# Performance work log

Hardware: AMD Instinct MI355X
Metric: run time of the kernel (lower is better)

## Reference

```python
import jax, jax.numpy as jnp
import numpy as np

IN_F = 4096
OUT_F = 4096
RANK = 8
ALPHA = 8
SCALE = ALPHA / RANK


def setup_inputs() -> dict:
    key = jax.random.key(0)
    kx, kw, kb, ka = jax.random.split(key, 4)
    x = jax.random.normal(kx, (4, 4096, IN_F), dtype=jnp.float32)
    # base frozen linear params (torch Linear default init style, any values ok)
    W = jax.random.normal(kw, (OUT_F, IN_F), dtype=jnp.float32) * (1.0 / np.sqrt(IN_F))
    b = jax.random.normal(kb, (OUT_F,), dtype=jnp.float32) * 0.01
    # lora_A: kaiming_uniform_(a=sqrt(5)) -> U(-bound, bound), bound = sqrt(6/((1+5)*in_f)) = 1/sqrt(in_f)
    bound = 1.0 / np.sqrt(IN_F)
    lora_A = jax.random.uniform(ka, (RANK, IN_F), dtype=jnp.float32, minval=-bound, maxval=bound)
    # lora_B initialized to zeros per module; use small random values so the LoRA path is exercised
    lora_B = jax.random.normal(jax.random.fold_in(key, 7), (OUT_F, RANK), dtype=jnp.float32) * 0.02
    return {"x": x, "W": W, "b": b, "lora_A": lora_A, "lora_B": lora_B}


def reference(x, W, b, lora_A, lora_B):
    # base: x @ W.T + b  [B,S,out_f]
    base = jnp.einsum("bsi,oi->bso", x, W) + b
    # low-rank path: (x @ A.T) @ B.T * scale
    xa = jnp.einsum("bsi,ri->bsr", x, lora_A)  # [B,S,r]
    lora = jnp.einsum("bsr,or->bso", xa, lora_B)
    return base + lora * SCALE
```

## Files before the change

kernel.cpp:

```cpp
#include <hip/hip_runtime.h>
#include <cstdint>

#define K_IN   4096
#define N_OUT  4096
#define M_ROWS 16384
#define RANK   8
#define LSCALE 1.0f
#define NT     64
#define ROWB   8192
#define AHALF  1048576

typedef __attribute__((ext_vector_type(8))) short  short8;
typedef __attribute__((ext_vector_type(4))) float  floatx4;

__device__ __forceinline__ unsigned short f2bf(float f) {
  uint32_t u = __float_as_uint(f);
  u += 0x7FFFu + ((u >> 16) & 1u);
  return (unsigned short)(u >> 16);
}

__global__ __launch_bounds__(256) void fold_w_kernel(
    const float* __restrict__ W, const float* __restrict__ lA,
    const float* __restrict__ lB, unsigned short* __restrict__ Weff) {
  int idx = blockIdx.x * 256 + threadIdx.x;
  int o = idx >> 10;
  int k = (idx & 1023) << 2;
  float4 w = *reinterpret_cast<const float4*>(W + (size_t)o * K_IN + k);
#pragma unroll
  for (int r = 0; r < RANK; ++r) {
    float s = LSCALE * lB[o * RANK + r];
    float4 a = *reinterpret_cast<const float4*>(lA + r * K_IN + k);
    w.x += s * a.x; w.y += s * a.y; w.z += s * a.z; w.w += s * a.w;
  }
  ushort4 p;
  p.x = f2bf(w.x); p.y = f2bf(w.y); p.z = f2bf(w.z); p.w = f2bf(w.w);
  *reinterpret_cast<ushort4*>(Weff + (size_t)o * K_IN + k) = p;
}

__global__ __launch_bounds__(256) void cvt_x_kernel(
    const float* __restrict__ x, unsigned short* __restrict__ xb) {
  size_t i = ((size_t)blockIdx.x * 256 + threadIdx.x) * 8;
  float4 a = *reinterpret_cast<const float4*>(x + i);
  float4 c = *reinterpret_cast<const float4*>(x + i + 4);
  uint4 v;
  v.x = (uint32_t)f2bf(a.x) | ((uint32_t)f2bf(a.y) << 16);
  v.y = (uint32_t)f2bf(a.z) | ((uint32_t)f2bf(a.w) << 16);
  v.z = (uint32_t)f2bf(c.x) | ((uint32_t)f2bf(c.y) << 16);
  v.w = (uint32_t)f2bf(c.z) | ((uint32_t)f2bf(c.w) << 16);
  *reinterpret_cast<uint4*>(xb + i) = v;
}

__device__ __forceinline__ void gload_lds16(const void* g, void* l) {
  __builtin_amdgcn_global_load_lds(
      (const __attribute__((address_space(1))) void*)g,
      (__attribute__((address_space(3))) void*)l, 16, 0, 0);
}

#define BAR() do { asm volatile("" ::: "memory");                         \
    __builtin_amdgcn_s_barrier();                                         \
    asm volatile("" ::: "memory"); } while (0)

#define DSR(DST, ADDR, IMM)                                               \
  asm volatile("ds_read_b128 %0, %1 offset:%2"                            \
               : "=v"(DST) : "v"(ADDR), "i"(IMM))
#define LGKM(N) do {                                                      \
    asm volatile("s_waitcnt lgkmcnt(" #N ")" ::: "memory");               \
    __builtin_amdgcn_sched_barrier(0); } while (0)
#define VMW(N) do {                                                       \
    asm volatile("s_waitcnt vmcnt(" #N ")" ::: "memory");                 \
    __builtin_amdgcn_sched_barrier(0); } while (0)

__global__ __launch_bounds__(512, 2) void gemm256_kernel(
    const unsigned short* __restrict__ Xb, const unsigned short* __restrict__ Wb,
    const float* __restrict__ bias, float* __restrict__ out) {
  __shared__ alignas(16) char lds[2 * 65536];

  const int tid  = threadIdx.x;
  const int wave = tid >> 6, lane = tid & 63;
  const int wr = wave >> 2, wc = wave & 3;
  const int l15 = lane & 15, sq = lane >> 4;

  int bx  = blockIdx.x;
  int sbx = (bx & 7) * 128 + (bx >> 3);
  const int mt = sbx >> 4;
  const int nt = sbx & 15;

  const int rstg = tid >> 3;
  const int cbst = (((tid & 7) ^ ((tid >> 3) & 7)) << 4);
  const char* aBase = (const char*)Xb + (size_t)(mt * 256 + rstg) * ROWB + cbst;
  const char* bBase = (const char*)Wb + (size_t)(nt * 256 + rstg) * ROWB + cbst;

#define STAGE_TH(TH, HH) do {                                             \
    const char* src_ = ((HH) < 2 ? aBase + (size_t)(HH) * AHALF           \
                                 : bBase + (size_t)((HH) - 2) * AHALF)    \
                       + (TH) * 128;                                      \
    char* dst_ = lds + ((TH) & 1) * 65536 + (HH) * 16384 + tid * 16;      \
    gload_lds16(src_, dst_);                                              \
    gload_lds16(src_ + (size_t)64 * ROWB, dst_ + 8192);                   \
  } while (0)

  const unsigned ldsb = (unsigned)(unsigned long long)
      (__attribute__((address_space(3))) char*)lds;
  const unsigned X = (unsigned)((l15 & 7) << 4);
  const unsigned aRow = ldsb + wr * 16384 + l15 * 128;
  const unsigned bRow = ldsb + (2 + (wc >> 1)) * 16384 + (wc & 1) * 8192
                        + l15 * 128;
  unsigned aCur0 = aRow + ((0u  + sq * 16) ^ X);
  unsigned aCur1 = aRow + ((64u + sq * 16) ^ X);
  unsigned bCur0 = bRow + ((0u  + sq * 16) ^ X);
  unsigned bCur1 = bRow + ((64u + sq * 16) ^ X);

#define LOAD_A(DST, MQ) do {                                              \
    _Pragma("unroll")                                                     \
    for (int fi = 0; fi < 4; ++fi)                                        \
      DSR(DST[fi],     aCur0, (MQ) * 8192 + fi * 2048);                   \
    _Pragma("unroll")                                                     \
    for (int fi = 0; fi < 4; ++fi)                                        \
      DSR(DST[4 + fi], aCur1, (MQ) * 8192 + fi * 2048);                   \
  } while (0)
#define LOAD_B4(DST, NQ) do {                                             \
    DSR(DST[0], bCur0, (NQ) * 4096);                                      \
    DSR(DST[1], bCur0, (NQ) * 4096 + 2048);                               \
    DSR(DST[2], bCur1, (NQ) * 4096);                                      \
    DSR(DST[3], bCur1, (NQ) * 4096 + 2048);                               \
  } while (0)
#define MFMA_Q(MQ, NQ, AF, BF) do {                                       \
    __builtin_amdgcn_s_setprio(1);                                        \
    _Pragma("unroll")                                                     \
    for (int ks = 0; ks < 2; ++ks)                                        \
      _Pragma("unroll")                                                   \
      for (int fi = 0; fi < 4; ++fi)                                      \
        _Pragma("unroll")                                                 \
        for (int fj = 0; fj < 2; ++fj)                                    \
          acc[(MQ) * 4 + fi][(NQ) * 2 + fj] =                             \
              __builtin_amdgcn_mfma_f32_16x16x32_bf16(                    \
                  AF[ks * 4 + fi], BF[ks * 2 + fj],                       \
                  acc[(MQ) * 4 + fi][(NQ) * 2 + fj], 0, 0, 0);            \
    __builtin_amdgcn_s_setprio(0); } while (0)

  floatx4 acc[8][4];
#pragma unroll
  for (int i = 0; i < 8; ++i)
#pragma unroll
    for (int j = 0; j < 4; ++j)
      acc[i][j] = (floatx4){0.f, 0.f, 0.f, 0.f};

  STAGE_TH(0, 0); STAGE_TH(0, 1); STAGE_TH(0, 2); STAGE_TH(0, 3);
  STAGE_TH(1, 0); STAGE_TH(1, 1); STAGE_TH(1, 2);
  VMW(6);
  BAR();

  short8 afA[8], afB[8], bfC[4], bfD[4];
  LOAD_A(afA, 0);
  LOAD_B4(bfC, 0);

  for (int t = 0; t < NT; ++t) {
    if (t <= NT - 2) STAGE_TH(t + 1, 3);
    LOAD_B4(bfD, 1);
    LOAD_A(afB, 1);
    LGKM(12);
    MFMA_Q(0, 0, afA, bfC);
    BAR();

    if (t <= NT - 3) STAGE_TH(t + 2, 0);
    LGKM(8);
    MFMA_Q(0, 1, afA, bfD);
    BAR();

    if (t <= NT - 3) STAGE_TH(t + 2, 1);
    LGKM(0);
    MFMA_Q(1, 0, afB, bfC);
    if (t <= NT - 3)      VMW(4);
    else if (t == NT - 2) VMW(0);
    BAR();

    if (t <= NT - 3) STAGE_TH(t + 2, 2);
    if (t <= NT - 2) {
      aCur0 ^= 65536u; aCur1 ^= 65536u; bCur0 ^= 65536u; bCur1 ^= 65536u;
      LOAD_A(afA, 0);
      LOAD_B4(bfC, 0);
    }
    __builtin_amdgcn_sched_barrier(0);
    MFMA_Q(1, 1, afB, bfD);
    BAR();
  }
#undef STAGE_TH
#undef LOAD_A
#undef LOAD_B4
#undef MFMA_Q

  const int row0 = mt * 256 + wr * 128 + sq * 4;
  const int col0 = nt * 256 + wc * 64 + l15;
#pragma unroll
  for (int j = 0; j < 4; ++j) {
    int col = col0 + j * 16;
    float bv = bias[col];
#pragma unroll
    for (int i = 0; i < 8; ++i) {
      int rowb = row0 + i * 16;
#pragma unroll
      for (int rr = 0; rr < 4; ++rr)
        out[(size_t)(rowb + rr) * N_OUT + col] = acc[i][j][rr] + bv;
    }
  }
}

__global__ __launch_bounds__(256) void fallback_kernel(
    const float* __restrict__ x, const float* __restrict__ W,
    const float* __restrict__ bias, const float* __restrict__ lA,
    const float* __restrict__ lB, float* __restrict__ out) {
  __shared__ float Xs[64][17];
  __shared__ float Ws[64][17];
  int tid = threadIdx.x;
  int tx = tid & 15, ty = tid >> 4;
  int bm = blockIdx.y * 64, bn = blockIdx.x * 64;
  float acc[4][4] = {};
  for (int k0 = 0; k0 < K_IN; k0 += 16) {
#pragma unroll
    for (int q = 0; q < 4; ++q) {
      int flat = q * 256 + tid;
      int r = flat >> 4, c = flat & 15;
      Xs[r][c] = x[(size_t)(bm + r) * K_IN + k0 + c];
      float w = W[(size_t)(bn + r) * K_IN + k0 + c];
#pragma unroll
      for (int rr = 0; rr < RANK; ++rr)
        w += LSCALE * lB[(bn + r) * RANK + rr] * lA[rr * K_IN + k0 + c];
      Ws[r][c] = w;
    }
    __syncthreads();
#pragma unroll
    for (int kk = 0; kk < 16; ++kk) {
      float av[4], bv[4];
#pragma unroll
      for (int i = 0; i < 4; ++i) av[i] = Xs[ty * 4 + i][kk];
#pragma unroll
      for (int j = 0; j < 4; ++j) bv[j] = Ws[tx * 4 + j][kk];
#pragma unroll
      for (int i = 0; i < 4; ++i)
#pragma unroll
        for (int j = 0; j < 4; ++j) acc[i][j] += av[i] * bv[j];
    }
    __syncthreads();
  }
#pragma unroll
  for (int i = 0; i < 4; ++i)
#pragma unroll
    for (int j = 0; j < 4; ++j)
      out[(size_t)(bm + ty * 4 + i) * N_OUT + bn + tx * 4 + j] =
          acc[i][j] + bias[bn + tx * 4 + j];
}

extern "C" void kernel_launch(void* const* d_in, const int* in_sizes, int n_in,
                              void* d_out, int out_size, void* d_ws, size_t ws_size,
                              hipStream_t stream) {
  const float* x  = (const float*)d_in[0];
  const float* W  = (const float*)d_in[1];
  const float* b  = (const float*)d_in[2];
  const float* lA = (const float*)d_in[3];
  const float* lB = (const float*)d_in[4];
  float* out = (float*)d_out;

  const size_t weff_bytes = (size_t)N_OUT * K_IN * 2;
  const size_t xb_bytes   = (size_t)M_ROWS * K_IN * 2;

  if (ws_size >= weff_bytes + xb_bytes) {
    unsigned short* Weff = (unsigned short*)d_ws;
    unsigned short* Xb   = (unsigned short*)((char*)d_ws + weff_bytes);
    fold_w_kernel<<<(int)(((size_t)N_OUT * K_IN / 4) / 256), 256, 0, stream>>>(W, lA, lB, Weff);
    cvt_x_kernel<<<(int)(((size_t)M_ROWS * K_IN / 8) / 256), 256, 0, stream>>>(x, Xb);
    gemm256_kernel<<<(M_ROWS / 256) * (N_OUT / 256), 512, 0, stream>>>(Xb, Weff, b, out);
  } else {
    dim3 grid(N_OUT / 64, M_ROWS / 64);
    fallback_kernel<<<grid, 256, 0, stream>>>(x, W, b, lA, lB, out);
  }
}
```

Before: 580.5 us.

## Switch GEMM mainloop to triple-buffered BK=32 stages with two barriers per tile

Measured after the change: 621.9 us. 1.07x slower.

```diff
diff --git a/kernel.cpp b/kernel.cpp
--- a/kernel.cpp
+++ b/kernel.cpp
@@ -6,9 +6,8 @@
 #define M_ROWS 16384
 #define RANK   8
 #define LSCALE 1.0f
-#define NT     64
+#define NT     128
 #define ROWB   8192
-#define AHALF  1048576
 
 typedef __attribute__((ext_vector_type(8))) short  short8;
 typedef __attribute__((ext_vector_type(4))) float  floatx4;
@@ -73,7 +72,7 @@
 __global__ __launch_bounds__(512, 2) void gemm256_kernel(
     const unsigned short* __restrict__ Xb, const unsigned short* __restrict__ Wb,
     const float* __restrict__ bias, float* __restrict__ out) {
-  __shared__ alignas(16) char lds[2 * 65536];
+  __shared__ alignas(16) char lds[3 * 32768];
 
   const int tid  = threadIdx.x;
   const int wave = tid >> 6, lane = tid & 63;
@@ -85,58 +84,57 @@
   const int mt = sbx >> 4;
   const int nt = sbx & 15;
 
-  const int rstg = tid >> 3;
-  const int cbst = (((tid & 7) ^ ((tid >> 3) & 7)) << 4);
-  const char* aBase = (const char*)Xb + (size_t)(mt * 256 + rstg) * ROWB + cbst;
-  const char* bBase = (const char*)Wb + (size_t)(nt * 256 + rstg) * ROWB + cbst;
-
-#define STAGE_TH(TH, HH) do {                                             \
-    const char* src_ = ((HH) < 2 ? aBase + (size_t)(HH) * AHALF           \
-                                 : bBase + (size_t)((HH) - 2) * AHALF)    \
-                       + (TH) * 128;                                      \
-    char* dst_ = lds + ((TH) & 1) * 65536 + (HH) * 16384 + tid * 16;      \
-    gload_lds16(src_, dst_);                                              \
-    gload_lds16(src_ + (size_t)64 * ROWB, dst_ + 8192);                   \
+  const int rstg = tid >> 2;
+  const int cbst = (((tid & 3) ^ ((tid >> 3) & 3)) << 4);
+  const char* aStage = (const char*)Xb + (size_t)(mt * 256 + rstg) * ROWB + cbst;
+  const char* bStage = (const char*)Wb + (size_t)(nt * 256 + rstg) * ROWB + cbst;
+
+#define STAGE_A(TT, STB) do {                                             \
+    const char* s_ = aStage + (TT) * 64;                                  \
+    char* d_ = lds + (STB) + tid * 16;                                    \
+    gload_lds16(s_, d_);                                                  \
+    gload_lds16(s_ + (size_t)128 * ROWB, d_ + 8192);                      \
+  } while (0)
+#define STAGE_B(TT, STB) do {                                             \
+    const char* s_ = bStage + (TT) * 64;                                  \
+    char* d_ = lds + (STB) + 16384 + tid * 16;                            \
+    gload_lds16(s_, d_);                                                  \
+    gload_lds16(s_ + (size_t)128 * ROWB, d_ + 8192);                      \
   } while (0)
 
   const unsigned ldsb = (unsigned)(unsigned long long)
       (__attribute__((address_space(3))) char*)lds;
-  const unsigned X = (unsigned)((l15 & 7) << 4);
-  const unsigned aRow = ldsb + wr * 16384 + l15 * 128;
-  const unsigned bRow = ldsb + (2 + (wc >> 1)) * 16384 + (wc & 1) * 8192
-                        + l15 * 128;
-  unsigned aCur0 = aRow + ((0u  + sq * 16) ^ X);
-  unsigned aCur1 = aRow + ((64u + sq * 16) ^ X);
-  unsigned bCur0 = bRow + ((0u  + sq * 16) ^ X);
-  unsigned bCur1 = bRow + ((64u + sq * 16) ^ X);
-
-#define LOAD_A(DST, MQ) do {                                              \
+  const unsigned swz = (unsigned)((sq * 16) ^ (((l15 >> 1) & 3) << 4));
+  const unsigned aBaseR = ldsb + wr * 8192 + l15 * 64 + swz;
+  const unsigned bBaseR = ldsb + 16384 + wc * 4096 + l15 * 64 + swz;
+
+#define LOAD_AFB(AD) do {                         \
+    DSR(afB[0], AD, 4096);                                                \
+    DSR(afB[1], AD, 4096 + 1024);                                         \
+    DSR(afB[2], AD, 4096 + 2048);                                         \
+    DSR(afB[3], AD, 4096 + 3072);                                         \
+  } while (0)
+#define LOAD_NXT(AFA, BFC, BFD, AD, BD) do {                              \
+    DSR(AFA[0], AD, 0);                                                   \
+    DSR(AFA[1], AD, 1024);                                                \
+    DSR(AFA[2], AD, 2048);                                                \
+    DSR(AFA[3], AD, 3072);                                                \
+    DSR(BFC[0], BD, 0);                                                   \
+    DSR(BFC[1], BD, 1024);                                                \
+    DSR(BFD[0], BD, 2048);                                                \
+    DSR(BFD[1], BD, 2048 + 1024);                                         \
+  } while (0)
+#define MFMA_Q(MQ, NQ, AF, BF) do {                                       \
     _Pragma("unroll")                                                     \
     for (int fi = 0; fi < 4; ++fi)                                        \
-      DSR(DST[fi],     aCur0, (MQ) * 8192 + fi * 2048);                   \
-    _Pragma("unroll")                                                     \
-    for (int fi = 0; fi < 4; ++fi)                                        \
-      DSR(DST[4 + fi], aCur1, (MQ) * 8192 + fi * 2048);                   \
-  } while (0)
-#define LOAD_B4(DST, NQ) do {                                             \
-    DSR(DST[0], bCur0, (NQ) * 4096);                                      \
-    DSR(DST[1], bCur0, (NQ) * 4096 + 2048);                               \
-    DSR(DST[2], bCur1, (NQ) * 4096);                                      \
-    DSR(DST[3], bCur1, (NQ) * 4096 + 2048);                               \
-  } while (0)
-#define MFMA_Q(MQ, NQ, AF, BF) do {                                       \
-    __builtin_amdgcn_s_setprio(1);                                        \
-    _Pragma("unroll")                                                     \
-    for (int ks = 0; ks < 2; ++ks)                                        \
       _Pragma("unroll")                                                   \
-      for (int fi = 0; fi < 4; ++fi)                                      \
-        _Pragma("unroll")                                                 \
-        for (int fj = 0; fj < 2; ++fj)                                    \
-          acc[(MQ) * 4 + fi][(NQ) * 2 + fj] =                             \
-              __builtin_amdgcn_mfma_f32_16x16x32_bf16(                    \
-                  AF[ks * 4 + fi], BF[ks * 2 + fj],                       \
-                  acc[(MQ) * 4 + fi][(NQ) * 2 + fj], 0, 0, 0);            \
-    __builtin_amdgcn_s_setprio(0); } while (0)
+      for (int fj = 0; fj < 2; ++fj)                                      \
+        acc[(MQ) * 4 + fi][(NQ) * 2 + fj] =                               \
+            __builtin_amdgcn_mfma_f32_16x16x32_bf16(                      \
+                AF[fi], BF[fj], acc[(MQ) * 4 + fi][(NQ) * 2 + fj],        \
+                0, 0, 0);                                                 \
+  } while (0)
+#define NEXTB(B) ((B) == 65536u ? 0u : (B) + 32768u)
 
   floatx4 acc[8][4];
 #pragma unroll
@@ -145,49 +143,56 @@
     for (int j = 0; j < 4; ++j)
       acc[i][j] = (floatx4){0.f, 0.f, 0.f, 0.f};
 
-  STAGE_TH(0, 0); STAGE_TH(0, 1); STAGE_TH(0, 2); STAGE_TH(0, 3);
-  STAGE_TH(1, 0); STAGE_TH(1, 1); STAGE_TH(1, 2);
-  VMW(6);
+  STAGE_A(0, 0u); STAGE_B(0, 0u);
+  STAGE_A(1, 32768u); STAGE_B(1, 32768u);
+  VMW(4);
   BAR();
 
-  short8 afA[8], afB[8], bfC[4], bfD[4];
-  LOAD_A(afA, 0);
-  LOAD_B4(bfC, 0);
-
-  for (int t = 0; t < NT; ++t) {
-    if (t <= NT - 2) STAGE_TH(t + 1, 3);
-    LOAD_B4(bfD, 1);
-    LOAD_A(afB, 1);
-    LGKM(12);
-    MFMA_Q(0, 0, afA, bfC);
-    BAR();
-
-    if (t <= NT - 3) STAGE_TH(t + 2, 0);
-    LGKM(8);
-    MFMA_Q(0, 1, afA, bfD);
-    BAR();
-
-    if (t <= NT - 3) STAGE_TH(t + 2, 1);
-    LGKM(0);
-    MFMA_Q(1, 0, afB, bfC);
-    if (t <= NT - 3)      VMW(4);
-    else if (t == NT - 2) VMW(0);
-    BAR();
-
-    if (t <= NT - 3) STAGE_TH(t + 2, 2);
-    if (t <= NT - 2) {
-      aCur0 ^= 65536u; aCur1 ^= 65536u; bCur0 ^= 65536u; bCur1 ^= 65536u;
-      LOAD_A(afA, 0);
-      LOAD_B4(bfC, 0);
-    }
-    __builtin_amdgcn_sched_barrier(0);
-    MFMA_Q(1, 1, afB, bfD);
-    BAR();
-  }
-#undef STAGE_TH
-#undef LOAD_A
-#undef LOAD_B4
+  short8 afA0[4], bfC0[2], bfD0[2];
+  short8 afA1[4], bfC1[2], bfD1[2];
+  short8 afB[4];
+  LOAD_NXT(afA0, bfC0, bfD0, aBaseR + 0u, bBaseR + 0u);
+
+  unsigned bR = 0u;
+
+#define TILE_BODY(T, AFAc, BFCc, BFDc, AFAn, BFCn, BFDn) do {             \
+    const unsigned bR1 = NEXTB(bR), bR2 = NEXTB(bR1);                     \
+                                                             \
+    LOAD_AFB(aBaseR + bR);                                                \
+    if ((T) <= NT - 3) STAGE_A((T) + 2, bR2);                             \
+    LGKM(4);                               \
+    __builtin_amdgcn_s_setprio(1);                                        \
+    MFMA_Q(0, 0, AFAc, BFCc);                                             \
+    MFMA_Q(0, 1, AFAc, BFDc);                                             \
+    __builtin_amdgcn_s_setprio(0);                                        \
+    if ((T) <= NT - 3)      VMW(2);         \
+    else if ((T) == NT - 2) VMW(0);                  \
+    BAR();                                     \
+                                                             \
+    if ((T) <= NT - 2)                                                    \
+      LOAD_NXT(AFAn, BFCn, BFDn, aBaseR + bR1, bBaseR + bR1);             \
+    if ((T) <= NT - 3) STAGE_B((T) + 2, bR2);                             \
+    if ((T) <= NT - 2) LGKM(8);          \
+    else               LGKM(0);                \
+    __builtin_amdgcn_s_setprio(1);                                        \
+    MFMA_Q(1, 0, afB, BFCc);                                              \
+    MFMA_Q(1, 1, afB, BFDc);                                              \
+    __builtin_amdgcn_s_setprio(0);                                        \
+    BAR();                                                                \
+    bR = bR1;                                                             \
+  } while (0)
+
+  for (int t = 0; t < NT; t += 2) {
+    TILE_BODY(t,     afA0, bfC0, bfD0, afA1, bfC1, bfD1);
+    TILE_BODY(t + 1, afA1, bfC1, bfD1, afA0, bfC0, bfD0);
+  }
+#undef TILE_BODY
+#undef STAGE_A
+#undef STAGE_B
+#undef LOAD_AFB
+#undef LOAD_NXT
 #undef MFMA_Q
+#undef NEXTB
 
   const int row0 = mt * 256 + wr * 128 + sq * 4;
   const int col0 = nt * 256 + wc * 64 + l15;
```
